# Kernel optimization log

Measured on AMD Instinct MI355X. Metric: run time of the kernel, lower is better.

## Reference

```python
import jax, jax.numpy as jnp
import numpy as np
import math

N_ITERS = 10
N_SPIXELS = 256
NEG_INF = -1e10


def _grid_layout(h, w, n_spixels):
    # init_grid: near-square superpixel grid
    nw = int(math.sqrt(n_spixels * w / h))
    nh = int(math.sqrt(n_spixels * h / w))
    cy = np.minimum((np.arange(h) * nh) // h, nh - 1)
    cx = np.minimum((np.arange(w) * nw) // w, nw - 1)
    iy = np.broadcast_to(cy[:, None], (h, w))
    ix = np.broadcast_to(cx[None, :], (h, w))
    init_idx = iy * nw + ix  # [h,w] hard grid assignment
    # 9 candidate superpixels per pixel (3x3 neighborhood of its grid cell)
    offs = np.array([(dy, dx) for dy in (-1, 0, 1) for dx in (-1, 0, 1)])
    ny = iy[None] + offs[:, 0, None, None]  # [9,h,w]
    nx = ix[None] + offs[:, 1, None, None]
    valid = (ny >= 0) & (ny < nh) & (nx >= 0) & (nx < nw)
    nidx = np.clip(ny, 0, nh - 1) * nw + np.clip(nx, 0, nw - 1)
    return init_idx.astype(np.int32), nidx.astype(np.int32), valid, nw, nh


def setup_inputs() -> dict:
    key = jax.random.key(0)
    x = jax.random.normal(key, (2, 20, 512, 512), dtype=jnp.float32)
    return {"x": x}


def reference(x):
    b, c, h, w = x.shape
    init_idx_np, nidx_np, valid_np, nw, nh = _grid_layout(h, w, N_SPIXELS)
    K = nw * nh
    n = h * w
    init_idx = jnp.asarray(init_idx_np.reshape(n))          # [N]
    nidx = jnp.asarray(nidx_np.reshape(9, n))                # [9,N]
    valid = jnp.asarray(valid_np.reshape(9, n))              # [9,N]
    flat_nidx = nidx.reshape(-1)                             # [9N]

    pf_all = x.reshape(b, c, n)

    def init_spf(pf):  # pf [c,N] -> [c,K]: hard-assignment mean (InitSpixelFeats)
        s = jax.ops.segment_sum(pf.T, init_idx, num_segments=K)      # [K,c]
        cnt = jax.ops.segment_sum(jnp.ones((n,), pf.dtype), init_idx, num_segments=K)
        return (s / jnp.maximum(cnt, 1.0)[:, None]).T

    def calc_neg_dist(pf, spf):  # CalcAssoc: [9,N] neg sq dist to 9 neighbors
        nf = spf[:, nidx]                                    # [c,9,N]
        d = jnp.sum((pf[:, None, :] - nf) ** 2, axis=0)      # [9,N]
        return jnp.where(valid, -d, NEG_INF)

    def map_p2sp(pf, Q):  # CalcSpixelFeats: Q-weighted scatter mean, Q [9,N]
        wf = (pf[:, None, :] * Q[None]).reshape(c, -1)       # [c,9N]
        num = jax.ops.segment_sum(wf.T, flat_nidx, num_segments=K)   # [K,c]
        den = jax.ops.segment_sum(Q.reshape(-1), flat_nidx, num_segments=K)
        return (num / jnp.maximum(den, 1e-8)[:, None]).T

    def per_sample(pf):
        spf0 = init_spf(jax.lax.stop_gradient(pf))  # spf init from detached pf
        Q0 = jnp.zeros((9, n), pf.dtype)
        def body(carry, _):
            spf, _ = carry
            Q = jax.nn.softmax(calc_neg_dist(pf, spf), axis=0)
            return (map_p2sp(pf, Q), Q), None
        (spf, Q), _ = jax.lax.scan(body, (spf0, Q0), None, length=N_ITERS)
        return Q, spf

    Q, spf = jax.vmap(per_sample)(pf_all)
    return Q.reshape(b, 9, h, w), spf, x
```

## Files before the change

kernel.cpp:

```cpp
#include <hip/hip_runtime.h>

#define BATCH 2
#define C 20
#define H 512
#define W 512
#define NPIX (H*W)
#define NW 16
#define NH 16
#define K 256
#define NITERS 10
#define SPLIT 4
#define PITCH 260
#define NEG_INF_F (-1.0e10f)
#define PART_STRIDE 189

__global__ void ssn_init_kernel(const float* __restrict__ x,
                                float* __restrict__ spf0) {
    int bi = blockIdx.x;
    int ch = bi % C;
    int k  = (bi / C) % K;
    int b  = bi / (C * K);
    int ky = k >> 4, kx = k & 15;
    const float* src = x + ((size_t)(b * C + ch)) * NPIX;
    int l = threadIdx.x;
    float s = 0.f;
#pragma unroll
    for (int i = 0; i < 16; ++i) {
        int p = l + 64 * i;
        int y = ky * 32 + (p >> 5);
        int xx = kx * 32 + (p & 31);
        s += src[y * W + xx];
    }
#pragma unroll
    for (int o = 32; o > 0; o >>= 1) s += __shfl_down(s, o);
    if (l == 0) spf0[(b * K + k) * C + ch] = s * (1.0f / 1024.0f);
}

__global__ void ssn_iterate_kernel(const float* __restrict__ x,
                                   const float* __restrict__ spf0,
                                   const float* __restrict__ rpart,
                                   float* __restrict__ wpart,
                                   float* __restrict__ outQ,
                                   float* __restrict__ outX,
                                   int iter, int last) {
    __shared__ float spf_lds[9][C];
    __shared__ float pf_tile[C][PITCH];
    __shared__ float w_tile[9][PITCH];

    int t = threadIdx.x;
    int bi = blockIdx.x;
    int s    = bi & 3;
    int cell = (bi >> 2) & (K - 1);
    int b    = bi >> 10;
    int ky = cell >> 4, kx = cell & 15;

    if (t < 9 * C) {
        int jj = t / C, ch = t % C;
        int ny = ky + jj / 3 - 1, nx = kx + jj % 3 - 1;
        float v = 0.f;
        if (ny >= 0 && ny < NH && nx >= 0 && nx < NW) {
            int cell2 = ny * NW + nx;
            if (iter == 0) {
                v = spf0[(b * K + cell2) * C + ch];
            } else {
                float num = 0.f, den = 0.f;
#pragma unroll
                for (int j2 = 0; j2 < 9; ++j2) {
                    int cy = ny - (j2 / 3 - 1), cx = nx - (j2 % 3 - 1);
                    if (cy >= 0 && cy < NH && cx >= 0 && cx < NW) {
                        const float* p = rpart +
                            (size_t)(b * K + cy * NW + cx) * (SPLIT * PART_STRIDE)
                            + j2 * 21;
#pragma unroll
                        for (int ss = 0; ss < SPLIT; ++ss) {
                            num += p[ss * PART_STRIDE + ch];
                            den += p[ss * PART_STRIDE + 20];
                        }
                    }
                }
                v = num / fmaxf(den, 1e-8f);
            }
        }
        spf_lds[jj][ch] = v;
    }
    __syncthreads();

    int py = t >> 5, px = t & 31;
    int y  = ky * 32 + s * 8 + py;
    int xx = kx * 32 + px;

    float pf[C];
    const float* xb = x + (size_t)b * C * NPIX + y * W + xx;
#pragma unroll
    for (int ch = 0; ch < C; ++ch) pf[ch] = xb[(size_t)ch * NPIX];

    float nd[9];
#pragma unroll
    for (int j = 0; j < 9; ++j) {
        int ny = ky + j / 3 - 1, nx = kx + j % 3 - 1;
        bool valid = (ny >= 0 && ny < NH && nx >= 0 && nx < NW);
        float d = 0.f;
#pragma unroll
        for (int ch = 0; ch < C; ++ch) {
            float df = pf[ch] - spf_lds[j][ch];
            d += df * df;
        }
        nd[j] = valid ? -d : NEG_INF_F;
    }
    float m = nd[0];
#pragma unroll
    for (int j = 1; j < 9; ++j) m = fmaxf(m, nd[j]);
    float wv[9], wsum = 0.f;
#pragma unroll
    for (int j = 0; j < 9; ++j) { wv[j] = __expf(nd[j] - m); wsum += wv[j]; }
    float inv = 1.0f / wsum;
#pragma unroll
    for (int j = 0; j < 9; ++j) { wv[j] *= inv; w_tile[j][t] = wv[j]; }
#pragma unroll
    for (int ch = 0; ch < C; ++ch) pf_tile[ch][t] = pf[ch];

    if (last) {
        float* q = outQ + (size_t)b * 9 * NPIX + y * W + xx;
#pragma unroll
        for (int j = 0; j < 9; ++j) q[(size_t)j * NPIX] = wv[j];
        float* ox = outX + (size_t)b * C * NPIX + y * W + xx;
#pragma unroll
        for (int ch = 0; ch < C; ++ch) ox[(size_t)ch * NPIX] = pf[ch];
    }
    __syncthreads();

    if (t < PART_STRIDE) {
        int j = t / 21, r = t % 21;
        const float4* wt = (const float4*)&w_tile[j][0];
        float acc = 0.f;
        if (r < 20) {
            const float4* pt = (const float4*)&pf_tile[r][0];
#pragma unroll 4
            for (int p = 0; p < 64; ++p) {
                float4 w4 = wt[p];
                float4 f4 = pt[p];
                acc += w4.x * f4.x + w4.y * f4.y + w4.z * f4.z + w4.w * f4.w;
            }
        } else {
#pragma unroll 4
            for (int p = 0; p < 64; ++p) {
                float4 w4 = wt[p];
                acc += w4.x + w4.y + w4.z + w4.w;
            }
        }
        wpart[(size_t)(b * K + cell) * (SPLIT * PART_STRIDE)
              + s * PART_STRIDE + t] = acc;
    }
}

__global__ void ssn_finalize_kernel(const float* __restrict__ part,
                                    float* __restrict__ outSpf) {
    int idx = blockIdx.x * blockDim.x + threadIdx.x;
    if (idx >= BATCH * K * C) return;
    int ch = idx % C;
    int k  = (idx / C) % K;
    int b  = idx / (C * K);
    int ky = k >> 4, kx = k & 15;
    float num = 0.f, den = 0.f;
#pragma unroll
    for (int j2 = 0; j2 < 9; ++j2) {
        int cy = ky - (j2 / 3 - 1), cx = kx - (j2 % 3 - 1);
        if (cy >= 0 && cy < NH && cx >= 0 && cx < NW) {
            const float* p = part +
                (size_t)(b * K + cy * NW + cx) * (SPLIT * PART_STRIDE) + j2 * 21;
#pragma unroll
            for (int ss = 0; ss < SPLIT; ++ss) {
                num += p[ss * PART_STRIDE + ch];
                den += p[ss * PART_STRIDE + 20];
            }
        }
    }
    outSpf[(b * C + ch) * K + k] = num / fmaxf(den, 1e-8f);
}

extern "C" void kernel_launch(void* const* d_in, const int* in_sizes, int n_in,
                              void* d_out, int out_size, void* d_ws, size_t ws_size,
                              hipStream_t stream) {
    const float* x = (const float*)d_in[0];
    float* out = (float*)d_out;
    float* outQ   = out;
    float* outSpf = out + (size_t)BATCH * 9 * NPIX;
    float* outX   = outSpf + (size_t)BATCH * C * K;

    float* ws    = (float*)d_ws;
    float* spf0  = ws;
    float* part0 = spf0 + (size_t)BATCH * K * C;
    float* part1 = part0 + (size_t)BATCH * K * SPLIT * PART_STRIDE;

    ssn_init_kernel<<<BATCH * K * C, 64, 0, stream>>>(x, spf0);

    for (int it = 0; it < NITERS; ++it) {
        const float* rp = (it % 2 == 0) ? part0 : part1;
        float*       wp = (it % 2 == 0) ? part1 : part0;
        ssn_iterate_kernel<<<BATCH * K * SPLIT, 256, 0, stream>>>(
            x, spf0, rp, wp, outQ, outX, it, (it == NITERS - 1) ? 1 : 0);
    }
    ssn_finalize_kernel<<<(BATCH * K * C + 255) / 256, 256, 0, stream>>>(part0, outSpf);
}
```

Baseline: 260.6 us.

## Split spf reduction into separate kernel and use dot-product distance

Moves the per-iteration reduction of partial sums into a dedicated small kernel that writes compact superpixel features. Each iterate block then loads only 180 values instead of redoing the 9x9x4 partial gathers per thread. The squared distance is rewritten as 2*dot minus the feature's squared norm, dropping the pixel norm, which is constant across candidates and cancels in the softmax. The x passthrough output becomes a device memcpy instead of per-thread stores in the last iteration. This adds nine extra kernel launches and slightly changes floating-point rounding.

```diff
diff --git a/kernel.cpp b/kernel.cpp
--- a/kernel.cpp
+++ b/kernel.cpp
@@ -36,14 +36,43 @@
     if (l == 0) spf0[(b * K + k) * C + ch] = s * (1.0f / 1024.0f);
 }
 
-__global__ void ssn_iterate_kernel(const float* __restrict__ x,
-                                   const float* __restrict__ spf0,
-                                   const float* __restrict__ rpart,
-                                   float* __restrict__ wpart,
-                                   float* __restrict__ outQ,
-                                   float* __restrict__ outX,
-                                   int iter, int last) {
+__global__ void ssn_reduce_kernel(const float* __restrict__ part,
+                                  float* __restrict__ spf,
+                                  float* __restrict__ outSpf,
+                                  int final_mode) {
+    int idx = blockIdx.x * blockDim.x + threadIdx.x;
+    if (idx >= BATCH * K * C) return;
+    int ch = idx % C;
+    int k  = (idx / C) % K;
+    int b  = idx / (C * K);
+    int ky = k >> 4, kx = k & 15;
+    float num = 0.f, den = 0.f;
+#pragma unroll
+    for (int j2 = 0; j2 < 9; ++j2) {
+        int cy = ky - (j2 / 3 - 1), cx = kx - (j2 % 3 - 1);
+        if (cy >= 0 && cy < NH && cx >= 0 && cx < NW) {
+            const float* p = part +
+                (size_t)(b * K + cy * NW + cx) * (SPLIT * PART_STRIDE) + j2 * 21;
+#pragma unroll
+            for (int ss = 0; ss < SPLIT; ++ss) {
+                num += p[ss * PART_STRIDE + ch];
+                den += p[ss * PART_STRIDE + 20];
+            }
+        }
+    }
+    float v = num / fmaxf(den, 1e-8f);
+    if (final_mode) outSpf[(b * C + ch) * K + k] = v;
+    else            spf[(b * K + k) * C + ch]    = v;
+}
+
+__global__ __launch_bounds__(256)
+void ssn_iterate_kernel(const float* __restrict__ x,
+                        const float* __restrict__ spf,
+                        float* __restrict__ wpart,
+                        float* __restrict__ outQ,
+                        int last) {
     __shared__ float spf_lds[9][C];
+    __shared__ float sumsq_lds[9];
     __shared__ float pf_tile[C][PITCH];
     __shared__ float w_tile[9][PITCH];
 
@@ -58,30 +87,19 @@
         int jj = t / C, ch = t % C;
         int ny = ky + jj / 3 - 1, nx = kx + jj % 3 - 1;
         float v = 0.f;
+        if (ny >= 0 && ny < NH && nx >= 0 && nx < NW)
+            v = spf[(size_t)(b * K + ny * NW + nx) * C + ch];
+        spf_lds[jj][ch] = v;
+    }
+    if (t < 9) {
+        int ny = ky + t / 3 - 1, nx = kx + t % 3 - 1;
+        float ss2 = 0.f;
         if (ny >= 0 && ny < NH && nx >= 0 && nx < NW) {
-            int cell2 = ny * NW + nx;
-            if (iter == 0) {
-                v = spf0[(b * K + cell2) * C + ch];
-            } else {
-                float num = 0.f, den = 0.f;
+            const float* sp = spf + (size_t)(b * K + ny * NW + nx) * C;
 #pragma unroll
-                for (int j2 = 0; j2 < 9; ++j2) {
-                    int cy = ny - (j2 / 3 - 1), cx = nx - (j2 % 3 - 1);
-                    if (cy >= 0 && cy < NH && cx >= 0 && cx < NW) {
-                        const float* p = rpart +
-                            (size_t)(b * K + cy * NW + cx) * (SPLIT * PART_STRIDE)
-                            + j2 * 21;
-#pragma unroll
-                        for (int ss = 0; ss < SPLIT; ++ss) {
-                            num += p[ss * PART_STRIDE + ch];
-                            den += p[ss * PART_STRIDE + 20];
-                        }
-                    }
-                }
-                v = num / fmaxf(den, 1e-8f);
-            }
+            for (int ch = 0; ch < C; ++ch) ss2 += sp[ch] * sp[ch];
         }
-        spf_lds[jj][ch] = v;
+        sumsq_lds[t] = ss2;
     }
     __syncthreads();
 
@@ -94,25 +112,22 @@
 #pragma unroll
     for (int ch = 0; ch < C; ++ch) pf[ch] = xb[(size_t)ch * NPIX];
 
-    float nd[9];
+    float sc[9];
 #pragma unroll
     for (int j = 0; j < 9; ++j) {
         int ny = ky + j / 3 - 1, nx = kx + j % 3 - 1;
         bool valid = (ny >= 0 && ny < NH && nx >= 0 && nx < NW);
-        float d = 0.f;
+        float dot = 0.f;
 #pragma unroll
-        for (int ch = 0; ch < C; ++ch) {
-            float df = pf[ch] - spf_lds[j][ch];
-            d += df * df;
-        }
-        nd[j] = valid ? -d : NEG_INF_F;
+        for (int ch = 0; ch < C; ++ch) dot = fmaf(pf[ch], spf_lds[j][ch], dot);
+        sc[j] = valid ? fmaf(2.f, dot, -sumsq_lds[j]) : NEG_INF_F;
     }
-    float m = nd[0];
+    float m = sc[0];
 #pragma unroll
-    for (int j = 1; j < 9; ++j) m = fmaxf(m, nd[j]);
+    for (int j = 1; j < 9; ++j) m = fmaxf(m, sc[j]);
     float wv[9], wsum = 0.f;
 #pragma unroll
-    for (int j = 0; j < 9; ++j) { wv[j] = __expf(nd[j] - m); wsum += wv[j]; }
+    for (int j = 0; j < 9; ++j) { wv[j] = __expf(sc[j] - m); wsum += wv[j]; }
     float inv = 1.0f / wsum;
 #pragma unroll
     for (int j = 0; j < 9; ++j) { wv[j] *= inv; w_tile[j][t] = wv[j]; }
@@ -123,9 +138,6 @@
         float* q = outQ + (size_t)b * 9 * NPIX + y * W + xx;
 #pragma unroll
         for (int j = 0; j < 9; ++j) q[(size_t)j * NPIX] = wv[j];
-        float* ox = outX + (size_t)b * C * NPIX + y * W + xx;
-#pragma unroll
-        for (int ch = 0; ch < C; ++ch) ox[(size_t)ch * NPIX] = pf[ch];
     }
     __syncthreads();
 
@@ -153,31 +165,6 @@
     }
 }
 
-__global__ void ssn_finalize_kernel(const float* __restrict__ part,
-                                    float* __restrict__ outSpf) {
-    int idx = blockIdx.x * blockDim.x + threadIdx.x;
-    if (idx >= BATCH * K * C) return;
-    int ch = idx % C;
-    int k  = (idx / C) % K;
-    int b  = idx / (C * K);
-    int ky = k >> 4, kx = k & 15;
-    float num = 0.f, den = 0.f;
-#pragma unroll
-    for (int j2 = 0; j2 < 9; ++j2) {
-        int cy = ky - (j2 / 3 - 1), cx = kx - (j2 % 3 - 1);
-        if (cy >= 0 && cy < NH && cx >= 0 && cx < NW) {
-            const float* p = part +
-                (size_t)(b * K + cy * NW + cx) * (SPLIT * PART_STRIDE) + j2 * 21;
-#pragma unroll
-            for (int ss = 0; ss < SPLIT; ++ss) {
-                num += p[ss * PART_STRIDE + ch];
-                den += p[ss * PART_STRIDE + 20];
-            }
-        }
-    }
-    outSpf[(b * C + ch) * K + k] = num / fmaxf(den, 1e-8f);
-}
-
 extern "C" void kernel_launch(void* const* d_in, const int* in_sizes, int n_in,
                               void* d_out, int out_size, void* d_ws, size_t ws_size,
                               hipStream_t stream) {
@@ -187,18 +174,22 @@
     float* outSpf = out + (size_t)BATCH * 9 * NPIX;
     float* outX   = outSpf + (size_t)BATCH * C * K;
 
-    float* ws    = (float*)d_ws;
-    float* spf0  = ws;
-    float* part0 = spf0 + (size_t)BATCH * K * C;
-    float* part1 = part0 + (size_t)BATCH * K * SPLIT * PART_STRIDE;
+    float* ws   = (float*)d_ws;
+    float* spf  = ws;
+    float* part = spf + (size_t)BATCH * K * C;
 
-    ssn_init_kernel<<<BATCH * K * C, 64, 0, stream>>>(x, spf0);
+    hipMemcpyAsync(outX, x, sizeof(float) * (size_t)BATCH * C * NPIX,
+                   hipMemcpyDeviceToDevice, stream);
+
+    ssn_init_kernel<<<BATCH * K * C, 64, 0, stream>>>(x, spf);
 
     for (int it = 0; it < NITERS; ++it) {
-        const float* rp = (it % 2 == 0) ? part0 : part1;
-        float*       wp = (it % 2 == 0) ? part1 : part0;
         ssn_iterate_kernel<<<BATCH * K * SPLIT, 256, 0, stream>>>(
-            x, spf0, rp, wp, outQ, outX, it, (it == NITERS - 1) ? 1 : 0);
+            x, spf, part, outQ, (it == NITERS - 1) ? 1 : 0);
+        if (it < NITERS - 1)
+            ssn_reduce_kernel<<<(BATCH * K * C + 255) / 256, 256, 0, stream>>>(
+                part, spf, nullptr, 0);
     }
-    ssn_finalize_kernel<<<(BATCH * K * C + 255) / 256, 256, 0, stream>>>(part0, outSpf);
+    ssn_reduce_kernel<<<(BATCH * K * C + 255) / 256, 256, 0, stream>>>(
+        part, nullptr, outSpf, 1);
 }
```

Measured after the change: 273.1 us. 1.05x slower.
